# Performance work log

Hardware: AMD Instinct MI355X
Metric: run time of the kernel (lower is better)

Reference implementation:

```python
import jax, jax.numpy as jnp
import numpy as np

B, I, H = 8192, 1024, 1024


def setup_inputs() -> dict:
    key = jax.random.key(0)
    ks = jax.random.split(key, 11)
    s = 1.0 / np.sqrt(I + H)  # torch Linear default init scale
    return {
        "input": jax.random.normal(ks[0], (B, I), jnp.float32),
        "hidden_state": jax.random.normal(ks[1], (B, H), jnp.float32),
        "cell_state": jax.random.normal(ks[2], (B, H), jnp.float32),
        "W_f": jax.random.uniform(ks[3], (I + H, H), jnp.float32, -s, s),
        "b_f": jax.random.uniform(ks[4], (H,), jnp.float32, -s, s),
        "W_i": jax.random.uniform(ks[5], (I + H, H), jnp.float32, -s, s),
        "b_i": jax.random.uniform(ks[6], (H,), jnp.float32, -s, s),
        "W_c": jax.random.uniform(ks[7], (I + H, H), jnp.float32, -s, s),
        "b_c": jax.random.uniform(ks[8], (H,), jnp.float32, -s, s),
        "W_o": jax.random.uniform(ks[9], (I + H, H), jnp.float32, -s, s),
        "b_o": jax.random.uniform(ks[10], (H,), jnp.float32, -s, s),
    }


def reference(input, hidden_state, cell_state, W_f, b_f, W_i, b_i, W_c, b_c, W_o, b_o):
    # Classic LSTM cell (cell='LSTM' intended path):
    # combined = [x, h]; four gate GEMMs; fused elementwise gate combine.
    combined = jnp.concatenate([input, hidden_state], axis=1)  # [B, I+H]
    # One fused GEMM for all 4 gates (weights concatenated along output dim)
    W = jnp.concatenate([W_f, W_i, W_c, W_o], axis=1)          # [I+H, 4H]
    b = jnp.concatenate([b_f, b_i, b_c, b_o], axis=0)          # [4H]
    gates = combined @ W + b                                   # [B, 4H]
    f, i, c_dash, o = jnp.split(gates, 4, axis=1)
    f = jax.nn.sigmoid(f)
    i = jax.nn.sigmoid(i)
    o = jax.nn.sigmoid(o)
    new_cell = f * cell_state + i * jnp.tanh(c_dash)
    new_hidden = o * jnp.tanh(new_cell)
    return new_hidden, new_cell
```

## Files before the change

kernel.cpp:

```cpp
#include <hip/hip_runtime.h>
#include <hip/hip_bf16.h>
#include <cstdint>


#define BROWS 8192
#define IH    2048
#define HDIM  1024

typedef __bf16 bf16x4 __attribute__((ext_vector_type(4)));
typedef __bf16 bf16x8 __attribute__((ext_vector_type(8)));
typedef float  f32x4  __attribute__((ext_vector_type(4)));

__global__ void pack_A(const float* __restrict__ x, const float* __restrict__ hs,
                       __bf16* __restrict__ A) {
    const int tid = threadIdx.x;
    const size_t base = (size_t)blockIdx.x * 2048;
#pragma unroll
    for (int p = 0; p < 2; ++p) {
        size_t e = base + (size_t)p * 1024 + (size_t)tid * 4;
        int row = (int)(e >> 11);
        int col = (int)(e & 2047);
        const float* src = (col < 1024) ? (x + (size_t)row * 1024 + col)
                                        : (hs + (size_t)row * 1024 + (col - 1024));
        float4 v = *(const float4*)src;
        bf16x4 r;
        r[0] = (__bf16)v.x; r[1] = (__bf16)v.y; r[2] = (__bf16)v.z; r[3] = (__bf16)v.w;
        *(bf16x4*)(A + e) = r;
    }
}

__global__ void pack_W(const float* __restrict__ Wf, const float* __restrict__ Wi,
                       const float* __restrict__ Wc, const float* __restrict__ Wo,
                       __bf16* __restrict__ Wt) {
    __shared__ float tile[32][33];
    int b = blockIdx.x;
    const int g = b & 3; b >>= 2;
    const int nt = b & 31;
    const int kt = b >> 5;
    const int n0 = nt * 32, k0 = kt * 32;
    const float* W = (g == 0) ? Wf : (g == 1) ? Wi : (g == 2) ? Wc : Wo;
    const int tid = threadIdx.x;
    {
        const int k = tid >> 3, c = tid & 7;
        *(float4*)&tile[k][c * 4] = *(const float4*)&W[(size_t)(k0 + k) * HDIM + n0 + c * 4];
    }
    __syncthreads();
    {
        const int n = tid >> 3, kq = tid & 7;
        bf16x4 r;
#pragma unroll
        for (int j = 0; j < 4; ++j) r[j] = (__bf16)tile[kq * 4 + j][n];
        *(bf16x4*)&Wt[(size_t)(g * HDIM + n0 + n) * IH + k0 + kq * 4] = r;
    }
}

#define BM 128
#define BH 32
#define BK 64

__global__ void lstm_gemm(const __bf16* __restrict__ A,
                          const __bf16* __restrict__ Wt,
                          const float* __restrict__ cell,
                          const float* __restrict__ bF_, const float* __restrict__ bI_,
                          const float* __restrict__ bC_, const float* __restrict__ bO_,
                          float* __restrict__ out)
{
    __shared__ __bf16 As[BM * BK];
    __shared__ __bf16 Bs[4 * BH * BK];

    const int tid  = threadIdx.x;
    const int wave = tid >> 6;
    const int lane = tid & 63;
    const int quad = lane >> 4;
    const int l16  = lane & 15;
    const int wr   = wave >> 1;
    const int wc   = wave & 1;
    const int sw   = l16 & 7;

    const int m0 = blockIdx.y * BM;
    const int h0 = blockIdx.x * BH;

    const int lrow = lane >> 3;
    const int lk   = (((lane & 7) ^ (lrow & 7)) << 3);

    f32x4 acc[4][4] = {};

    for (int k0 = 0; k0 < IH; k0 += BK) {
#pragma unroll
        for (int i = 0; i < 4; ++i) {
            int c = wave * 4 + i;
            int row = c * 8 + lrow;
            const __bf16* gp = A + (size_t)(m0 + row) * IH + k0 + lk;
            __bf16* lp = &As[c * 8 * BK];
            __builtin_amdgcn_global_load_lds(
                (const __attribute__((address_space(1))) unsigned*)gp,
                (__attribute__((address_space(3))) unsigned*)lp, 16, 0, 0);
        }
#pragma unroll
        for (int i = 0; i < 4; ++i) {
            int c = wave * 4 + i;
            int rl = c * 8 + lrow;
            int g = rl >> 5, hl = rl & 31;
            const __bf16* gp = Wt + (size_t)(g * HDIM + h0 + hl) * IH + k0 + lk;
            __bf16* lp = &Bs[c * 8 * BK];
            __builtin_amdgcn_global_load_lds(
                (const __attribute__((address_space(1))) unsigned*)gp,
                (__attribute__((address_space(3))) unsigned*)lp, 16, 0, 0);
        }
        __syncthreads();

#pragma unroll
        for (int ki = 0; ki < BK; ki += 32) {
            const int kk = ki >> 3;
            const int ch = (kk + quad) ^ sw;
            bf16x8 af[4], bg[4];
#pragma unroll
            for (int r = 0; r < 4; ++r) {
                int ra = wr * 64 + r * 16 + l16;
                af[r] = *(const bf16x8*)&As[ra * BK + (ch << 3)];
            }
#pragma unroll
            for (int g = 0; g < 4; ++g) {
                int rb = g * 32 + wc * 16 + l16;
                bg[g] = *(const bf16x8*)&Bs[rb * BK + (ch << 3)];
            }
#pragma unroll
            for (int g = 0; g < 4; ++g)
#pragma unroll
                for (int r = 0; r < 4; ++r)
                    acc[g][r] = __builtin_amdgcn_mfma_f32_16x16x32_bf16(
                        af[r], bg[g], acc[g][r], 0, 0, 0);
        }
        __syncthreads();
    }

    const int h = h0 + wc * 16 + l16;
    const float bF = bF_[h], bI = bI_[h], bC = bC_[h], bO = bO_[h];
#pragma unroll
    for (int r = 0; r < 4; ++r) {
#pragma unroll
        for (int reg = 0; reg < 4; ++reg) {
            const int m = m0 + wr * 64 + r * 16 + quad * 4 + reg;
            float pf = acc[0][r][reg] + bF;
            float pi = acc[1][r][reg] + bI;
            float pc = acc[2][r][reg] + bC;
            float po = acc[3][r][reg] + bO;
            float f  = 1.f / (1.f + __expf(-pf));
            float ig = 1.f / (1.f + __expf(-pi));
            float og = 1.f / (1.f + __expf(-po));
            float e2 = __expf(2.f * pc);
            float cd = (e2 - 1.f) / (e2 + 1.f);
            float cp = cell[(size_t)m * HDIM + h];
            float cn = f * cp + ig * cd;
            float ec = __expf(2.f * cn);
            float tc = (ec - 1.f) / (ec + 1.f);
            out[(size_t)m * HDIM + h] = og * tc;
            out[(size_t)BROWS * HDIM + (size_t)m * HDIM + h] = cn;
        }
    }
}

extern "C" void kernel_launch(void* const* d_in, const int* in_sizes, int n_in,
                              void* d_out, int out_size, void* d_ws, size_t ws_size,
                              hipStream_t stream) {
    const float* x  = (const float*)d_in[0];
    const float* hs = (const float*)d_in[1];
    const float* cs = (const float*)d_in[2];
    const float* Wf = (const float*)d_in[3];
    const float* bF = (const float*)d_in[4];
    const float* Wi = (const float*)d_in[5];
    const float* bI = (const float*)d_in[6];
    const float* Wc = (const float*)d_in[7];
    const float* bC = (const float*)d_in[8];
    const float* Wo = (const float*)d_in[9];
    const float* bO = (const float*)d_in[10];
    float* out = (float*)d_out;

    __bf16* A  = (__bf16*)d_ws;
    __bf16* Wt = (__bf16*)((char*)d_ws + (size_t)BROWS * IH * 2);

    pack_A<<<BROWS * IH / 2048, 256, 0, stream>>>(x, hs, A);
    pack_W<<<4 * 32 * 64, 256, 0, stream>>>(Wf, Wi, Wc, Wo, Wt);
    lstm_gemm<<<dim3(HDIM / BH, BROWS / BM), 256, 0, stream>>>(A, Wt, cs, bF, bI, bC, bO, out);
}
```

Before: 314.6 us.

## Rewrite LSTM GEMM with 256x256 tiles, double-buffered LDS and interleaved prefetch

The fused gate GEMM now uses 512-thread blocks covering 256 rows by 64 hidden units (256 gate columns), with double-buffered dynamic LDS of 128 KB. Global-to-LDS loads for the next tiles are split into quarters and interleaved with MFMA phases under manual waitcnt, barriers and setprio. The aim is to hide memory latency and raise operand reuse per LDS load. In exchange it uses far more registers and LDS per block and relies on delicate hand-placed synchronisation.

```diff
diff --git a/kernel.cpp b/kernel.cpp
--- a/kernel.cpp
+++ b/kernel.cpp
@@ -54,97 +54,140 @@
     }
 }
 
-#define BM 128
-#define BH 32
-#define BK 64
-
-__global__ void lstm_gemm(const __bf16* __restrict__ A,
-                          const __bf16* __restrict__ Wt,
-                          const float* __restrict__ cell,
-                          const float* __restrict__ bF_, const float* __restrict__ bI_,
-                          const float* __restrict__ bC_, const float* __restrict__ bO_,
-                          float* __restrict__ out)
+
+#define BM  256
+#define BK  64
+#define NT  (IH / BK)
+#define ATB (BM * BK)
+
+__device__ __forceinline__ void gload16(const __bf16* g, __bf16* l) {
+    __builtin_amdgcn_global_load_lds(
+        (const __attribute__((address_space(1))) unsigned*)g,
+        (__attribute__((address_space(3))) unsigned*)l, 16, 0, 0);
+}
+
+#define LGKM0() do { asm volatile("s_waitcnt lgkmcnt(0)" ::: "memory"); \
+                     __builtin_amdgcn_sched_barrier(0); } while (0)
+#define VMC6()  asm volatile("s_waitcnt vmcnt(6)" ::: "memory")
+#define VMC0()  asm volatile("s_waitcnt vmcnt(0)" ::: "memory")
+#define BAR()   __builtin_amdgcn_s_barrier()
+
+#define SA(dst, T, rb) gload16(aA + (size_t)(rb) * IH + (size_t)(T) * BK, \
+                               (dst) + ((rb) + wv8) * BK)
+#define SB(dst, T, rb) gload16(bB + (size_t)(rb) * 32768 + (size_t)(T) * BK, \
+                               (dst) + ((rb) + wv8) * BK)
+#define ISS_AH0(dst, T) do { SA(dst, T, 0);   SA(dst, T, 128); } while (0)
+#define ISS_AH1(dst, T) do { SA(dst, T, 64);  SA(dst, T, 192); } while (0)
+#define ISS_BH0(dst, T) do { SB(dst, T, 0);   SB(dst, T, 64);  } while (0)
+#define ISS_BH1(dst, T) do { SB(dst, T, 128); SB(dst, T, 192); } while (0)
+
+#define LD_AF(MH, Ac) do { \
+    _Pragma("unroll") for (int m_ = 0; m_ < 4; ++m_) \
+    _Pragma("unroll") for (int ks_ = 0; ks_ < 2; ++ks_) \
+        af[m_][ks_] = *(const bf16x8*)&(Ac)[(wr128 + (MH) * 64 + m_ * 16 + l16) * BK \
+                                            + (((ks_ * 4 + quad) ^ sw) << 3)]; \
+} while (0)
+
+#define LD_BG(NH, Bc) do { \
+    _Pragma("unroll") for (int n_ = 0; n_ < 2; ++n_) \
+    _Pragma("unroll") for (int ks_ = 0; ks_ < 2; ++ks_) \
+        bg[(NH) * 2 + n_][ks_] = *(const bf16x8*)&(Bc)[(((NH) * 2 + n_) * 64 + wc16 + l16) * BK \
+                                                       + (((ks_ * 4 + quad) ^ sw) << 3)]; \
+} while (0)
+
+#define MFMA_Q(MH, NH) do { \
+    __builtin_amdgcn_s_setprio(1); \
+    _Pragma("unroll") for (int n_ = 0; n_ < 2; ++n_) \
+    _Pragma("unroll") for (int m_ = 0; m_ < 4; ++m_) \
+    _Pragma("unroll") for (int ks_ = 0; ks_ < 2; ++ks_) \
+        acc[(MH) * 4 + m_][(NH) * 2 + n_] = __builtin_amdgcn_mfma_f32_16x16x32_bf16( \
+            af[m_][ks_], bg[(NH) * 2 + n_][ks_], acc[(MH) * 4 + m_][(NH) * 2 + n_], 0, 0, 0); \
+    __builtin_amdgcn_s_setprio(0); \
+} while (0)
+
+#define TILE(T, Ac, Bc, An, ISS1, ISS2, VMW) do { \
+    LD_AF(0, Ac); LD_BG(0, Bc); \
+    if (ISS1) ISS_AH1(An, (T) + 1); \
+    BAR(); LGKM0(); \
+    MFMA_Q(0, 0); \
+    BAR(); \
+    LD_BG(1, Bc); \
+    if (ISS2) ISS_AH0(Ac, (T) + 2); \
+    BAR(); LGKM0(); \
+    MFMA_Q(0, 1); \
+    BAR(); \
+    LD_AF(1, Ac); \
+    if (ISS2) ISS_BH0(Bc, (T) + 2); \
+    BAR(); LGKM0(); \
+    MFMA_Q(1, 0); \
+    BAR(); \
+    if (ISS2) ISS_BH1(Bc, (T) + 2); \
+    BAR(); \
+    MFMA_Q(1, 1); \
+    if ((VMW) == 6) { VMC6(); } else if ((VMW) == 0) { VMC0(); } \
+    BAR(); \
+} while (0)
+
+__global__ __launch_bounds__(512, 2) void lstm_gemm(
+    const __bf16* __restrict__ A,
+    const __bf16* __restrict__ Wt,
+    const float* __restrict__ cell,
+    const float* __restrict__ bF_, const float* __restrict__ bI_,
+    const float* __restrict__ bC_, const float* __restrict__ bO_,
+    float* __restrict__ out)
 {
-    __shared__ __bf16 As[BM * BK];
-    __shared__ __bf16 Bs[4 * BH * BK];
+    extern __shared__ __bf16 lds[];
+    __bf16* Asb = lds;
+    __bf16* Bsb = lds + 2 * ATB;
 
     const int tid  = threadIdx.x;
     const int wave = tid >> 6;
     const int lane = tid & 63;
     const int quad = lane >> 4;
     const int l16  = lane & 15;
-    const int wr   = wave >> 1;
-    const int wc   = wave & 1;
     const int sw   = l16 & 7;
+    const int wr   = wave >> 2;
+    const int wc   = wave & 3;
+    const int lrow = lane >> 3;
+    const int lk   = ((lane & 7) ^ lrow) << 3;
+    const int wv8  = wave * 8;
+    const int wr128 = wr * 128;
+    const int wc16  = wc * 16;
 
     const int m0 = blockIdx.y * BM;
-    const int h0 = blockIdx.x * BH;
-
-    const int lrow = lane >> 3;
-    const int lk   = (((lane & 7) ^ (lrow & 7)) << 3);
-
-    f32x4 acc[4][4] = {};
-
-    for (int k0 = 0; k0 < IH; k0 += BK) {
-#pragma unroll
-        for (int i = 0; i < 4; ++i) {
-            int c = wave * 4 + i;
-            int row = c * 8 + lrow;
-            const __bf16* gp = A + (size_t)(m0 + row) * IH + k0 + lk;
-            __bf16* lp = &As[c * 8 * BK];
-            __builtin_amdgcn_global_load_lds(
-                (const __attribute__((address_space(1))) unsigned*)gp,
-                (__attribute__((address_space(3))) unsigned*)lp, 16, 0, 0);
-        }
-#pragma unroll
-        for (int i = 0; i < 4; ++i) {
-            int c = wave * 4 + i;
-            int rl = c * 8 + lrow;
-            int g = rl >> 5, hl = rl & 31;
-            const __bf16* gp = Wt + (size_t)(g * HDIM + h0 + hl) * IH + k0 + lk;
-            __bf16* lp = &Bs[c * 8 * BK];
-            __builtin_amdgcn_global_load_lds(
-                (const __attribute__((address_space(1))) unsigned*)gp,
-                (__attribute__((address_space(3))) unsigned*)lp, 16, 0, 0);
-        }
-        __syncthreads();
-
-#pragma unroll
-        for (int ki = 0; ki < BK; ki += 32) {
-            const int kk = ki >> 3;
-            const int ch = (kk + quad) ^ sw;
-            bf16x8 af[4], bg[4];
-#pragma unroll
-            for (int r = 0; r < 4; ++r) {
-                int ra = wr * 64 + r * 16 + l16;
-                af[r] = *(const bf16x8*)&As[ra * BK + (ch << 3)];
-            }
-#pragma unroll
-            for (int g = 0; g < 4; ++g) {
-                int rb = g * 32 + wc * 16 + l16;
-                bg[g] = *(const bf16x8*)&Bs[rb * BK + (ch << 3)];
-            }
-#pragma unroll
-            for (int g = 0; g < 4; ++g)
-#pragma unroll
-                for (int r = 0; r < 4; ++r)
-                    acc[g][r] = __builtin_amdgcn_mfma_f32_16x16x32_bf16(
-                        af[r], bg[g], acc[g][r], 0, 0, 0);
-        }
-        __syncthreads();
-    }
-
-    const int h = h0 + wc * 16 + l16;
-    const float bF = bF_[h], bI = bI_[h], bC = bC_[h], bO = bO_[h];
-#pragma unroll
-    for (int r = 0; r < 4; ++r) {
-#pragma unroll
-        for (int reg = 0; reg < 4; ++reg) {
-            const int m = m0 + wr * 64 + r * 16 + quad * 4 + reg;
-            float pf = acc[0][r][reg] + bF;
-            float pi = acc[1][r][reg] + bI;
-            float pc = acc[2][r][reg] + bC;
-            float po = acc[3][r][reg] + bO;
+    const int h0 = blockIdx.x * 64;
+
+    const __bf16* aA = A  + (size_t)(m0 + wv8 + lrow) * IH + lk;
+    const __bf16* bB = Wt + (size_t)(h0 + wv8 + lrow) * IH + lk;
+
+    f32x4 acc[8][4] = {};
+    bf16x8 af[4][2], bg[4][2];
+
+    ISS_AH0(Asb, 0); ISS_BH0(Bsb, 0); ISS_BH1(Bsb, 0); ISS_AH1(Asb, 0);
+    ISS_AH0(Asb + ATB, 1); ISS_BH0(Bsb + ATB, 1); ISS_BH1(Bsb + ATB, 1);
+    VMC6();
+    BAR();
+
+    for (int t = 0; t < NT - 2; ++t) {
+        __bf16* Ac = Asb + (t & 1) * ATB;
+        __bf16* Bc = Bsb + (t & 1) * ATB;
+        __bf16* An = Asb + ((t & 1) ^ 1) * ATB;
+        TILE(t, Ac, Bc, An, true, true, 6);
+    }
+    TILE(NT - 2, Asb, Bsb, Asb + ATB, true, false, 0);
+    TILE(NT - 1, Asb + ATB, Bsb + ATB, Asb, false, false, -1);
+
+    const int h = h0 + wc16 + l16;
+    const float bFv = bF_[h], bIv = bI_[h], bCv = bC_[h], bOv = bO_[h];
+#pragma unroll
+    for (int mi = 0; mi < 8; ++mi) {
+#pragma unroll
+        for (int r = 0; r < 4; ++r) {
+            const int m = m0 + wr128 + mi * 16 + quad * 4 + r;
+            float pf = acc[mi][0][r] + bFv;
+            float pi = acc[mi][1][r] + bIv;
+            float pc = acc[mi][2][r] + bCv;
+            float po = acc[mi][3][r] + bOv;
             float f  = 1.f / (1.f + __expf(-pf));
             float ig = 1.f / (1.f + __expf(-pi));
             float og = 1.f / (1.f + __expf(-po));
@@ -179,7 +222,10 @@
     __bf16* A  = (__bf16*)d_ws;
     __bf16* Wt = (__bf16*)((char*)d_ws + (size_t)BROWS * IH * 2);
 
+    (void)hipFuncSetAttribute((const void*)lstm_gemm,
+                              hipFuncAttributeMaxDynamicSharedMemorySize, 131072);
+
     pack_A<<<BROWS * IH / 2048, 256, 0, stream>>>(x, hs, A);
     pack_W<<<4 * 32 * 64, 256, 0, stream>>>(Wf, Wi, Wc, Wo, Wt);
-    lstm_gemm<<<dim3(HDIM / BH, BROWS / BM), 256, 0, stream>>>(A, Wt, cs, bF, bI, bC, bO, out);
-}
+    lstm_gemm<<<dim3(HDIM / 64, BROWS / BM), 512, 131072, stream>>>(A, Wt, cs, bF, bI, bC, bO, out);
+}
```

After: 313.1 us. No clear change (-0.5%).
